# Performance work log

Measured on AMD Instinct MI355X. Metric: run time of the kernel, lower is better.

## Reference

```python
import jax, jax.numpy as jnp
import numpy as np

IN_FEATURES = 8192
OUT_FEATURES = 8192
CODESZ = 8            # E8 lattice dimension per code index
CODEBOOK_SIZE = 65536 # 2^16-entry codebook (16-bit indices)
TOKENS = 32           # decode-style batch


def fwht(x):
    """Fast Walsh-Hadamard transform (Sylvester order) along the last axis.
    n must be a power of 2. Unnormalized (multiply by H_n)."""
    n = x.shape[-1]
    steps = int(np.log2(n))
    h = 1
    for _ in range(steps):
        y = x.reshape(*x.shape[:-1], n // (2 * h), 2, h)
        a = y[..., 0, :]
        b = y[..., 1, :]
        x = jnp.stack([a + b, a - b], axis=-2).reshape(*y.shape[:-3], n)
        h *= 2
    return x


def setup_inputs() -> dict:
    key = jax.random.key(0)
    k0, k1, k2, k3, k4 = jax.random.split(key, 5)
    x = jax.random.normal(k0, (TOKENS, IN_FEATURES), dtype=jnp.float32)
    # learned codebook: CODEBOOK_SIZE vectors of CODESZ entries (E8P-like lattice points)
    codebook_table = jax.random.normal(k1, (CODEBOOK_SIZE, CODESZ), dtype=jnp.float32) * 0.1
    # quantized weight indices: [out_features, in_features // codesz]
    Qidxs = jax.random.randint(k2, (OUT_FEATURES, IN_FEATURES // CODESZ), 0, CODEBOOK_SIZE, dtype=jnp.int32)
    # random sign vectors (incoherence processing)
    SU = (2.0 * jax.random.randint(k3, (IN_FEATURES,), 0, 2) - 1.0).astype(jnp.float32)
    SV = (2.0 * jax.random.randint(k4, (OUT_FEATURES,), 0, 2) - 1.0).astype(jnp.float32)
    Wscale = jnp.array(0.02, dtype=jnp.float32)
    return {"x": x, "codebook_table": codebook_table, "Qidxs": Qidxs,
            "SU": SU, "SV": SV, "Wscale": Wscale}


def reference(x, codebook_table, Qidxs, SU, SV, Wscale):
    n_in = x.shape[-1]
    n_out = SV.shape[0]
    # input incoherence: sign flip then orthonormal Hadamard rotation (matmul_hadUt)
    xh = fwht(x * SU) * (1.0 / jnp.sqrt(jnp.float32(n_in)))  # [T, n_in]
    # codebook dequantization: gather lattice vectors and lay out as [n_out, n_in]
    W = codebook_table[Qidxs].reshape(n_out, n_in)
    # quantized matmul in the rotated basis
    z = xh @ W.T  # [T, n_out]
    # output rotation (matmul_hadU) + sign/scale (SV absorbs Wscale in the torch code)
    out = fwht(z) * (1.0 / jnp.sqrt(jnp.float32(n_out))) * (SV * Wscale)
    return out
```

## Files before the change

kernel.cpp:

```cpp
#include <hip/hip_runtime.h>
#include <hip/hip_bf16.h>


typedef __attribute__((ext_vector_type(4))) float f32x4;
typedef __attribute__((ext_vector_type(16))) float f32x16;
typedef __attribute__((ext_vector_type(8))) __bf16 bf16x8;
typedef __attribute__((ext_vector_type(4))) __bf16 bf16x4;
typedef __attribute__((ext_vector_type(4))) int i32x4;

#define IN_F 8192
#define OUT_F 8192
#define TOKENS 32
#define KSPLIT 16
#define KCHUNK 512
#define NTILES (KCHUNK / 16)
#define NG (NTILES / 2)
#define DG 5
#define DI 7
#define CH (KCHUNK / 8)
#define INV_SQRT_8192 0.011048543456039806f
#define PAD(i) ((i) + ((i) >> 5))

__device__ inline void fwht32_reg(float* r) {
    #pragma unroll
    for (int h = 1; h < 32; h <<= 1)
        #pragma unroll
        for (int i = 0; i < 32; i += 2 * h)
            #pragma unroll
            for (int j = 0; j < h; ++j) {
                float a = r[i + j], b = r[i + j + h];
                r[i + j] = a + b;
                r[i + j + h] = a - b;
            }
}

__device__ inline void fwht8192_lds(float* s, int tid) {
    float r[32];
    int b1 = tid * 32;
    #pragma unroll
    for (int j = 0; j < 32; ++j) r[j] = s[PAD(b1 + j)];
    fwht32_reg(r);
    #pragma unroll
    for (int j = 0; j < 32; ++j) s[PAD(b1 + j)] = r[j];
    __syncthreads();
    int b2 = (tid & 31) + (tid >> 5) * 1024;
    #pragma unroll
    for (int j = 0; j < 32; ++j) r[j] = s[PAD(b2 + 32 * j)];
    fwht32_reg(r);
    #pragma unroll
    for (int j = 0; j < 32; ++j) s[PAD(b2 + 32 * j)] = r[j];
    __syncthreads();
    #pragma unroll
    for (int jj = 0; jj < 4; ++jj) {
        float g[8];
        int b3 = tid * 4 + jj;
        #pragma unroll
        for (int k = 0; k < 8; ++k) g[k] = s[PAD(b3 + 1024 * k)];
        #pragma unroll
        for (int h = 1; h < 8; h <<= 1)
            #pragma unroll
            for (int i = 0; i < 8; i += 2 * h)
                #pragma unroll
                for (int j = 0; j < h; ++j) {
                    float a = g[i + j], b = g[i + j + h];
                    g[i + j] = a + b;
                    g[i + j + h] = a - b;
                }
        #pragma unroll
        for (int k = 0; k < 8; ++k) s[PAD(b3 + 1024 * k)] = g[k];
    }
    __syncthreads();
}

__global__ __launch_bounds__(256)
void prep_kernel(const float* __restrict__ cb, __bf16* __restrict__ cbb,
                 const float* __restrict__ x, const float* __restrict__ su,
                 __bf16* __restrict__ xh) {
    __shared__ float s[8192 + 256];
    const int tid = threadIdx.x;
    if (blockIdx.x < 512) {
        int i = blockIdx.x * 256 + tid;
        float4 v = ((const float4*)cb)[i];
        bf16x4 o;
        o[0] = (__bf16)v.x; o[1] = (__bf16)v.y;
        o[2] = (__bf16)v.z; o[3] = (__bf16)v.w;
        ((bf16x4*)cbb)[i] = o;
        return;
    }
    const int t = blockIdx.x - 512;
    #pragma unroll
    for (int i = tid; i < IN_F; i += 256)
        s[PAD(i)] = x[t * IN_F + i] * su[i];
    __syncthreads();
    fwht8192_lds(s, tid);
    #pragma unroll
    for (int i = tid; i < IN_F; i += 256)
        xh[t * IN_F + i] = (__bf16)(s[PAD(i)] * INV_SQRT_8192);
}

__global__ __launch_bounds__(512, 4)
void qgemm_kernel(const int* __restrict__ qidxs,
                  const __bf16* __restrict__ cb,
                  const __bf16* __restrict__ xh,
                  __bf16* __restrict__ zpart) {
    __shared__ __align__(16) __bf16 xt[TOKENS * KCHUNK];
    const int ks = blockIdx.x & 15;
    const int nb = blockIdx.x >> 4;
    const int tid = threadIdx.x;
    const int wave = tid >> 6, lane = tid & 63;
    const int h = lane >> 5, lc = lane & 31;
    const int n = nb * 256 + wave * 32 + lc;

    #pragma unroll
    for (int i = 0; i < 4; ++i) {
        int f = i * 512 + tid, r = f >> 6, c = f & 63;
        i32x4 v = *(const i32x4*)(xh + (size_t)r * IN_F + ks * KCHUNK + c * 8);
        *(i32x4*)(xt + ((r * CH + (c ^ (r & 7))) << 3)) = v;
    }
    __syncthreads();

    const int* qrow = qidxs + (size_t)n * (IN_F / 8) + ks * CH;
    const bf16x8* cbv = (const bf16x8*)cb;

    f32x16 acc;
    #pragma unroll
    for (int i = 0; i < 16; ++i) acc[i] = 0.f;

    i32x4 iv[NG];
    bf16x8 bfr[NG][2];

    #pragma unroll
    for (int g = 0; g < DI; ++g)
        iv[g] = *(const i32x4*)(qrow + g * 4);
    #pragma unroll
    for (int g = 0; g < DG; ++g) {
        int e0 = h ? iv[g][1] : iv[g][0];
        int e1 = h ? iv[g][3] : iv[g][2];
        bfr[g][0] = cbv[e0];
        bfr[g][1] = cbv[e1];
    }

    #pragma unroll
    for (int g = 0; g < NG; ++g) {
        if (g + DI < NG)
            iv[g + DI] = *(const i32x4*)(qrow + (g + DI) * 4);
        if (g + DG < NG) {
            int e0 = h ? iv[g + DG][1] : iv[g + DG][0];
            int e1 = h ? iv[g + DG][3] : iv[g + DG][2];
            bfr[g + DG][0] = cbv[e0];
            bfr[g + DG][1] = cbv[e1];
        }
        #pragma unroll
        for (int s = 0; s < 2; ++s) {
            const int T = 2 * g + s;
            bf16x8 a = *(const bf16x8*)(xt +
                          ((lc * CH + ((2 * T + h) ^ (lc & 7))) << 3));
            acc = __builtin_amdgcn_mfma_f32_32x32x16_bf16(a, bfr[g][s], acc,
                                                          0, 0, 0);
        }
    }

    __bf16* zp = zpart + ((size_t)ks * TOKENS) * OUT_F + n;
    #pragma unroll
    for (int r = 0; r < 16; ++r) {
        int m = (r & 3) + 4 * h + 8 * (r >> 2);
        zp[(size_t)m * OUT_F] = (__bf16)acc[r];
    }
}

__global__ __launch_bounds__(256)
void zsum_kernel(const __bf16* __restrict__ zpart, const float* __restrict__ sv,
                 const float* __restrict__ wscale, float* __restrict__ out) {
    __shared__ float s[8192 + 256];
    const int t = blockIdx.x, tid = threadIdx.x;
    #pragma unroll
    for (int cc = 0; cc < 4; ++cc) {
        int col = cc * 2048 + tid * 8;
        float a[8] = {0.f, 0.f, 0.f, 0.f, 0.f, 0.f, 0.f, 0.f};
        #pragma unroll
        for (int ks = 0; ks < KSPLIT; ++ks) {
            bf16x8 v = *(const bf16x8*)(zpart +
                         ((size_t)(ks * TOKENS + t)) * OUT_F + col);
            #pragma unroll
            for (int j = 0; j < 8; ++j) a[j] += (float)v[j];
        }
        #pragma unroll
        for (int j = 0; j < 8; ++j) s[PAD(col + j)] = a[j];
    }
    __syncthreads();
    fwht8192_lds(s, tid);
    const float sc = INV_SQRT_8192 * wscale[0];
    #pragma unroll
    for (int i = tid; i < OUT_F; i += 256)
        out[t * OUT_F + i] = s[PAD(i)] * sc * sv[i];
}

extern "C" void kernel_launch(void* const* d_in, const int* in_sizes, int n_in,
                              void* d_out, int out_size, void* d_ws, size_t ws_size,
                              hipStream_t stream) {
    const float* x      = (const float*)d_in[0];
    const float* cb     = (const float*)d_in[1];
    const int*   qidxs  = (const int*)d_in[2];
    const float* su     = (const float*)d_in[3];
    const float* sv     = (const float*)d_in[4];
    const float* wscale = (const float*)d_in[5];
    float* out = (float*)d_out;

    char* ws = (char*)d_ws;
    __bf16* cb_bf16 = (__bf16*)ws;
    __bf16* xh      = (__bf16*)(ws + (1u << 20));
    __bf16* zpart   = (__bf16*)(ws + (1u << 20) + (512u << 10));

    hipLaunchKernelGGL(prep_kernel, dim3(544), dim3(256), 0, stream,
                       cb, cb_bf16, x, su, xh);
    hipLaunchKernelGGL(qgemm_kernel, dim3(32 * KSPLIT), dim3(512), 0, stream,
                       qidxs, cb_bf16, xh, zpart);
    hipLaunchKernelGGL(zsum_kernel, dim3(TOKENS), dim3(256), 0, stream,
                       zpart, sv, wscale, out);
}
```

Before: 139.0 us.

## Restructure qgemm inner loop into explicit software pipeline with ring buffers

Rewrites the qgemm main loop as a single software-pipelined loop. Index loads run DI=8 groups ahead, codebook gathers DG=6 ahead, and LDS A-fragments one ahead, all held in small ring buffers. Index loads now use nontemporal hints, and a sched_barrier keeps the MFMA issue separate from the loads. The goal is to hide gather and LDS latency behind MFMAs while using fewer registers. The deeper prefetch raises register pressure and may hurt occupancy, and the sched_barrier limits how freely the compiler can schedule.

```diff
diff --git a/kernel.cpp b/kernel.cpp
--- a/kernel.cpp
+++ b/kernel.cpp
@@ -15,8 +15,10 @@
 #define KCHUNK 512
 #define NTILES (KCHUNK / 16)
 #define NG (NTILES / 2)
-#define DG 5
-#define DI 7
+#define DG 6
+#define DI 8
+#define BB (DG + 1)
+#define BIV (DI - DG + 1)
 #define CH (KCHUNK / 8)
 #define INV_SQRT_8192 0.011048543456039806f
 #define PAD(i) ((i) + ((i) >> 5))
@@ -126,37 +128,33 @@
     #pragma unroll
     for (int i = 0; i < 16; ++i) acc[i] = 0.f;
 
-    i32x4 iv[NG];
-    bf16x8 bfr[NG][2];
-
-    #pragma unroll
-    for (int g = 0; g < DI; ++g)
-        iv[g] = *(const i32x4*)(qrow + g * 4);
-    #pragma unroll
-    for (int g = 0; g < DG; ++g) {
-        int e0 = h ? iv[g][1] : iv[g][0];
-        int e1 = h ? iv[g][3] : iv[g][2];
-        bfr[g][0] = cbv[e0];
-        bfr[g][1] = cbv[e1];
-    }
-
-    #pragma unroll
-    for (int g = 0; g < NG; ++g) {
-        if (g + DI < NG)
-            iv[g + DI] = *(const i32x4*)(qrow + (g + DI) * 4);
-        if (g + DG < NG) {
-            int e0 = h ? iv[g + DG][1] : iv[g + DG][0];
-            int e1 = h ? iv[g + DG][3] : iv[g + DG][2];
-            bfr[g + DG][0] = cbv[e0];
-            bfr[g + DG][1] = cbv[e1];
-        }
-        #pragma unroll
-        for (int s = 0; s < 2; ++s) {
-            const int T = 2 * g + s;
-            bf16x8 a = *(const bf16x8*)(xt +
-                          ((lc * CH + ((2 * T + h) ^ (lc & 7))) << 3));
-            acc = __builtin_amdgcn_mfma_f32_32x32x16_bf16(a, bfr[g][s], acc,
-                                                          0, 0, 0);
+    i32x4 iv[BIV];
+    bf16x8 bfr[BB][2];
+    bf16x8 areg[2][2];
+
+    #pragma unroll
+    for (int v = -DI; v < NG; ++v) {
+        if (v + DI < NG)
+            iv[(v + DI) % BIV] = __builtin_nontemporal_load(
+                (const i32x4*)(qrow + (v + DI) * 4));
+        if (v + DG >= 0 && v + DG < NG) {
+            i32x4 e = iv[(v + DG) % BIV];
+            bfr[(v + DG) % BB][0] = cbv[h ? e[1] : e[0]];
+            bfr[(v + DG) % BB][1] = cbv[h ? e[3] : e[2]];
+        }
+        if (v + 1 >= 0 && v + 1 < NG) {
+            const int T0 = 2 * (v + 1), T1 = T0 + 1;
+            areg[(v + 1) & 1][0] = *(const bf16x8*)(xt +
+                ((lc * CH + ((2 * T0 + h) ^ (lc & 7))) << 3));
+            areg[(v + 1) & 1][1] = *(const bf16x8*)(xt +
+                ((lc * CH + ((2 * T1 + h) ^ (lc & 7))) << 3));
+        }
+        __builtin_amdgcn_sched_barrier(0);
+        if (v >= 0) {
+            acc = __builtin_amdgcn_mfma_f32_32x32x16_bf16(
+                      areg[v & 1][0], bfr[v % BB][0], acc, 0, 0, 0);
+            acc = __builtin_amdgcn_mfma_f32_32x32x16_bf16(
+                      areg[v & 1][1], bfr[v % BB][1], acc, 0, 0, 0);
         }
     }
 
```

After: 149.9 us. 1.08x slower.

## Split each K chunk across two wave groups to double qgemm parallelism

Applied to the files above, without the earlier changes.

Adds a qgemm variant where each block covers 128 output columns, and its eight waves split the 512-wide K chunk into two halves. The grid grows to 1024 blocks and there are 32 partial-sum slices instead of 16. The reduction kernel is templated on the slice count and sums 32 slices. The index loads now use nontemporal hints. The goal is more blocks and occupancy to hide gather latency, at the cost of twice the partial-sum traffic in the reduction and a dependency on workspace size, with the old path kept as a fallback.

```diff
diff --git a/kernel.cpp b/kernel.cpp
--- a/kernel.cpp
+++ b/kernel.cpp
@@ -2,7 +2,6 @@
 #include <hip/hip_bf16.h>
 
 
-typedef __attribute__((ext_vector_type(4))) float f32x4;
 typedef __attribute__((ext_vector_type(16))) float f32x16;
 typedef __attribute__((ext_vector_type(8))) __bf16 bf16x8;
 typedef __attribute__((ext_vector_type(4))) __bf16 bf16x4;
@@ -11,13 +10,10 @@
 #define IN_F 8192
 #define OUT_F 8192
 #define TOKENS 32
-#define KSPLIT 16
 #define KCHUNK 512
-#define NTILES (KCHUNK / 16)
-#define NG (NTILES / 2)
+#define CH (KCHUNK / 8)
 #define DG 5
 #define DI 7
-#define CH (KCHUNK / 8)
 #define INV_SQRT_8192 0.011048543456039806f
 #define PAD(i) ((i) + ((i) >> 5))
 
@@ -99,10 +95,10 @@
 }
 
 __global__ __launch_bounds__(512, 4)
-void qgemm_kernel(const int* __restrict__ qidxs,
-                  const __bf16* __restrict__ cb,
-                  const __bf16* __restrict__ xh,
-                  __bf16* __restrict__ zpart) {
+void qgemm16_kernel(const int* __restrict__ qidxs,
+                    const __bf16* __restrict__ cb,
+                    const __bf16* __restrict__ xh,
+                    __bf16* __restrict__ zpart) {
     __shared__ __align__(16) __bf16 xt[TOKENS * KCHUNK];
     const int ks = blockIdx.x & 15;
     const int nb = blockIdx.x >> 4;
@@ -126,37 +122,34 @@
     #pragma unroll
     for (int i = 0; i < 16; ++i) acc[i] = 0.f;
 
-    i32x4 iv[NG];
-    bf16x8 bfr[NG][2];
+    i32x4 iv[16];
+    bf16x8 bfr[16][2];
 
     #pragma unroll
     for (int g = 0; g < DI; ++g)
-        iv[g] = *(const i32x4*)(qrow + g * 4);
+        iv[g] = __builtin_nontemporal_load((const i32x4*)(qrow + g * 4));
     #pragma unroll
     for (int g = 0; g < DG; ++g) {
-        int e0 = h ? iv[g][1] : iv[g][0];
-        int e1 = h ? iv[g][3] : iv[g][2];
-        bfr[g][0] = cbv[e0];
-        bfr[g][1] = cbv[e1];
-    }
-
-    #pragma unroll
-    for (int g = 0; g < NG; ++g) {
-        if (g + DI < NG)
-            iv[g + DI] = *(const i32x4*)(qrow + (g + DI) * 4);
-        if (g + DG < NG) {
-            int e0 = h ? iv[g + DG][1] : iv[g + DG][0];
-            int e1 = h ? iv[g + DG][3] : iv[g + DG][2];
-            bfr[g + DG][0] = cbv[e0];
-            bfr[g + DG][1] = cbv[e1];
-        }
-        #pragma unroll
-        for (int s = 0; s < 2; ++s) {
-            const int T = 2 * g + s;
+        bfr[g][0] = cbv[h ? iv[g][1] : iv[g][0]];
+        bfr[g][1] = cbv[h ? iv[g][3] : iv[g][2]];
+    }
+
+    #pragma unroll
+    for (int g = 0; g < 16; ++g) {
+        if (g + DI < 16)
+            iv[g + DI] = __builtin_nontemporal_load(
+                (const i32x4*)(qrow + (g + DI) * 4));
+        if (g + DG < 16) {
+            bfr[g + DG][0] = cbv[h ? iv[g + DG][1] : iv[g + DG][0]];
+            bfr[g + DG][1] = cbv[h ? iv[g + DG][3] : iv[g + DG][2]];
+        }
+        #pragma unroll
+        for (int sgi = 0; sgi < 2; ++sgi) {
+            const int T = 2 * g + sgi;
             bf16x8 a = *(const bf16x8*)(xt +
                           ((lc * CH + ((2 * T + h) ^ (lc & 7))) << 3));
-            acc = __builtin_amdgcn_mfma_f32_32x32x16_bf16(a, bfr[g][s], acc,
-                                                          0, 0, 0);
+            acc = __builtin_amdgcn_mfma_f32_32x32x16_bf16(a, bfr[g][sgi],
+                                                          acc, 0, 0, 0);
         }
     }
 
@@ -168,6 +161,76 @@
     }
 }
 
+__global__ __launch_bounds__(512, 8)
+void qgemm32_kernel(const int* __restrict__ qidxs,
+                    const __bf16* __restrict__ cb,
+                    const __bf16* __restrict__ xh,
+                    __bf16* __restrict__ zpart) {
+    __shared__ __align__(16) __bf16 xt[TOKENS * KCHUNK];
+    const int ks = blockIdx.x & 15;
+    const int nb = blockIdx.x >> 4;
+    const int tid = threadIdx.x;
+    const int wave = tid >> 6, lane = tid & 63;
+    const int ng = wave & 3, kh = wave >> 2;
+    const int h = lane >> 5, lc = lane & 31;
+    const int n = nb * 128 + ng * 32 + lc;
+
+    #pragma unroll
+    for (int i = 0; i < 4; ++i) {
+        int f = i * 512 + tid, r = f >> 6, c = f & 63;
+        i32x4 v = *(const i32x4*)(xh + (size_t)r * IN_F + ks * KCHUNK + c * 8);
+        *(i32x4*)(xt + ((r * CH + (c ^ (r & 7))) << 3)) = v;
+    }
+    __syncthreads();
+
+    const int* qrow = qidxs + (size_t)n * (IN_F / 8) + ks * CH + kh * 32;
+    const bf16x8* cbv = (const bf16x8*)cb;
+
+    f32x16 acc;
+    #pragma unroll
+    for (int i = 0; i < 16; ++i) acc[i] = 0.f;
+
+    i32x4 iv[8];
+    bf16x8 bfr[8][2];
+
+    #pragma unroll
+    for (int g = 0; g < DI; ++g)
+        iv[g] = __builtin_nontemporal_load((const i32x4*)(qrow + g * 4));
+    #pragma unroll
+    for (int g = 0; g < DG; ++g) {
+        bfr[g][0] = cbv[h ? iv[g][1] : iv[g][0]];
+        bfr[g][1] = cbv[h ? iv[g][3] : iv[g][2]];
+    }
+
+    #pragma unroll
+    for (int g = 0; g < 8; ++g) {
+        if (g + DI < 8)
+            iv[g + DI] = __builtin_nontemporal_load(
+                (const i32x4*)(qrow + (g + DI) * 4));
+        if (g + DG < 8) {
+            bfr[g + DG][0] = cbv[h ? iv[g + DG][1] : iv[g + DG][0]];
+            bfr[g + DG][1] = cbv[h ? iv[g + DG][3] : iv[g + DG][2]];
+        }
+        #pragma unroll
+        for (int sgi = 0; sgi < 2; ++sgi) {
+            const int T = kh * 16 + 2 * g + sgi;
+            bf16x8 a = *(const bf16x8*)(xt +
+                          ((lc * CH + ((2 * T + h) ^ (lc & 7))) << 3));
+            acc = __builtin_amdgcn_mfma_f32_32x32x16_bf16(a, bfr[g][sgi],
+                                                          acc, 0, 0, 0);
+        }
+    }
+
+    const int p = ks * 2 + kh;
+    __bf16* zp = zpart + ((size_t)p * TOKENS) * OUT_F + n;
+    #pragma unroll
+    for (int r = 0; r < 16; ++r) {
+        int m = (r & 3) + 4 * h + 8 * (r >> 2);
+        zp[(size_t)m * OUT_F] = (__bf16)acc[r];
+    }
+}
+
+template <int PIECES>
 __global__ __launch_bounds__(256)
 void zsum_kernel(const __bf16* __restrict__ zpart, const float* __restrict__ sv,
                  const float* __restrict__ wscale, float* __restrict__ out) {
@@ -178,9 +241,9 @@
         int col = cc * 2048 + tid * 8;
         float a[8] = {0.f, 0.f, 0.f, 0.f, 0.f, 0.f, 0.f, 0.f};
         #pragma unroll
-        for (int ks = 0; ks < KSPLIT; ++ks) {
+        for (int p = 0; p < PIECES; ++p) {
             bf16x8 v = *(const bf16x8*)(zpart +
-                         ((size_t)(ks * TOKENS + t)) * OUT_F + col);
+                         ((size_t)(p * TOKENS + t)) * OUT_F + col);
             #pragma unroll
             for (int j = 0; j < 8; ++j) a[j] += (float)v[j];
         }
@@ -213,8 +276,18 @@
 
     hipLaunchKernelGGL(prep_kernel, dim3(544), dim3(256), 0, stream,
                        cb, cb_bf16, x, su, xh);
-    hipLaunchKernelGGL(qgemm_kernel, dim3(32 * KSPLIT), dim3(512), 0, stream,
-                       qidxs, cb_bf16, xh, zpart);
-    hipLaunchKernelGGL(zsum_kernel, dim3(TOKENS), dim3(256), 0, stream,
-                       zpart, sv, wscale, out);
-}
+
+    const size_t need32 = (1u << 20) + (512u << 10) +
+                          (size_t)32 * TOKENS * OUT_F * 2;
+    if (ws_size >= need32) {
+        hipLaunchKernelGGL(qgemm32_kernel, dim3(1024), dim3(512), 0, stream,
+                           qidxs, cb_bf16, xh, zpart);
+        hipLaunchKernelGGL((zsum_kernel<32>), dim3(TOKENS), dim3(256), 0,
+                           stream, zpart, sv, wscale, out);
+    } else {
+        hipLaunchKernelGGL(qgemm16_kernel, dim3(512), dim3(512), 0, stream,
+                           qidxs, cb_bf16, xh, zpart);
+        hipLaunchKernelGGL((zsum_kernel<16>), dim3(TOKENS), dim3(256), 0,
+                           stream, zpart, sv, wscale, out);
+    }
+}
```

Result: slower. 159.4 us (+14.7%).
